# Kernel tuning notes

Measured on AMD Instinct MI355X. Metric: run time of the kernel, lower is better.

## Reference

```python
import jax, jax.numpy as jnp
import numpy as np

L, H, E, HS, T, B, V, BS = 12, 12, 768, 64, 1024, 4, 50257, 1024
EPS = 1e-8
SCALE = E ** -0.5  # NOTE: original code scales by n_embd**-0.5, not head_size**-0.5


def _ln(x, g, b):
    mu = jnp.mean(x, axis=-1, keepdims=True)
    var = jnp.mean((x - mu) ** 2, axis=-1, keepdims=True)
    return (x - mu) / jnp.sqrt(var + EPS) * g + b


def setup_inputs() -> dict:
    key = jax.random.key(0)
    ks = iter(jax.random.split(key, 32))
    s = 0.02
    inp = {
        "idx": jax.random.randint(next(ks), (B, T), 0, V, dtype=jnp.int64),
        "tok_emb": jax.random.normal(next(ks), (V, E), jnp.float32) * s,
        "pos_emb": jax.random.normal(next(ks), (BS, E), jnp.float32) * s,
        "wq": jax.random.normal(next(ks), (L, H, E, HS), jnp.float32) * s,
        "wk": jax.random.normal(next(ks), (L, H, E, HS), jnp.float32) * s,
        "wv": jax.random.normal(next(ks), (L, H, E, HS), jnp.float32) * s,
        "proj_w": jax.random.normal(next(ks), (L, E, E), jnp.float32) * s,
        "proj_b": jnp.zeros((L, E), jnp.float32),
        "ln1_g": jnp.ones((L, E), jnp.float32),
        "ln1_b": jnp.zeros((L, E), jnp.float32),
        "ln2_g": jnp.ones((L, E), jnp.float32),
        "ln2_b": jnp.zeros((L, E), jnp.float32),
        "w1": jax.random.normal(next(ks), (L, E, 4 * E), jnp.float32) * s,
        "b1": jnp.zeros((L, 4 * E), jnp.float32),
        "w2": jax.random.normal(next(ks), (L, 4 * E, E), jnp.float32) * s,
        "b2": jnp.zeros((L, E), jnp.float32),
        "lnf_g": jnp.ones((E,), jnp.float32),
        "lnf_b": jnp.zeros((E,), jnp.float32),
        "head_w": jax.random.normal(next(ks), (E, V), jnp.float32) * s,
        "head_b": jnp.zeros((V,), jnp.float32),
    }
    return inp


def reference(idx, tok_emb, pos_emb, wq, wk, wv, proj_w, proj_b,
              ln1_g, ln1_b, ln2_g, ln2_b, w1, b1, w2, b2,
              lnf_g, lnf_b, head_w, head_b):
    x = tok_emb[idx] + pos_emb[jnp.arange(T)][None, :, :]  # [B,T,E]
    mask = jnp.tril(jnp.ones((T, T), bool))
    neg = jnp.finfo(x.dtype).min
    for l in range(L):
        # --- multi-head attention ---
        xn = _ln(x, ln1_g[l], ln1_b[l])
        q = jnp.einsum("bte,hed->bhtd", xn, wq[l])
        k = jnp.einsum("bte,hed->bhtd", xn, wk[l])
        v = jnp.einsum("bte,hed->bhtd", xn, wv[l])
        scores = jnp.einsum("bhtd,bhsd->bhts", q, k) * SCALE
        scores = jnp.where(mask, scores, neg)
        attn = jax.nn.softmax(scores, axis=-1)
        o = jnp.einsum("bhts,bhsd->bhtd", attn, v)  # [B,H,T,HS]
        o = o.transpose(0, 2, 1, 3).reshape(B, T, E)
        x = x + o @ proj_w[l].T + proj_b[l]
        # --- feed-forward ---
        xn = _ln(x, ln2_g[l], ln2_b[l])
        h = jax.nn.gelu(xn @ w1[l] + b1[l], approximate=False)
        x = x + h @ w2[l] + b2[l]
    x = _ln(x, lnf_g, lnf_b)
    logits = x @ head_w + head_b  # [B,T,V]
    return logits
```

## Files before the change

### kernel.cpp

```cpp
#include <hip/hip_runtime.h>
#include <hip/hip_bf16.h>
#include <stdint.h>
#include <math.h>

typedef __hip_bfloat16 bf16;
typedef short s16x8 __attribute__((ext_vector_type(8)));
typedef short s16x4 __attribute__((ext_vector_type(4)));
typedef float f32x4 __attribute__((ext_vector_type(4)));

#define SCALE_QK 0.03608439182435161f
#define NEG_BIG  -1.0e30f

__device__ __forceinline__ void lds_dma16(void* lds_uniform, const void* gsrc) {
  __builtin_amdgcn_global_load_lds(
      (const __attribute__((address_space(1))) unsigned int*)(uintptr_t)gsrc,
      (__attribute__((address_space(3))) unsigned int*)(unsigned int)(uintptr_t)lds_uniform,
      16, 0, 0);
}

enum { EPI_BF16 = 0, EPI_GELU = 1, EPI_RES = 2, EPI_HEAD = 3 };

template <int EPI>
__global__ __launch_bounds__(256)
void gemm_bt(const bf16* __restrict__ A, const bf16* __restrict__ BT,
             const float* __restrict__ bias, float* Cf, bf16* Cb,
             int M, int N, int K, int Nreal)
{
  __shared__ __align__(16) bf16 As[2][128 * 32];
  __shared__ __align__(16) bf16 Bs[2][128 * 32];
  const int tid = threadIdx.x;
  const int w = tid >> 6, l = tid & 63;
  const int lo = l & 15, hi = l >> 4;
  const int wm = (w & 1) * 64, wn = (w >> 1) * 64;
  const long row0 = (long)blockIdx.y * 128;
  const long col0 = (long)blockIdx.x * 128;

  const int c0 = w * 64 + l, c1 = c0 + 256;
  const bf16* a0 = A + (row0 + (c0 >> 2)) * K + (c0 & 3) * 8;
  const bf16* a1 = A + (row0 + (c1 >> 2)) * K + (c1 & 3) * 8;
  const bf16* b0 = BT + (col0 + (c0 >> 2)) * K + (c0 & 3) * 8;
  const bf16* b1 = BT + (col0 + (c1 >> 2)) * K + (c1 & 3) * 8;
  const int w512 = w * 512;

  const f32x4 zero4 = {0.f, 0.f, 0.f, 0.f};
  f32x4 acc[4][4];
#pragma unroll
  for (int m = 0; m < 4; ++m)
#pragma unroll
    for (int n = 0; n < 4; ++n) acc[m][n] = zero4;

  const int nk = K >> 5;
  lds_dma16(&As[0][w512],        a0);
  lds_dma16(&As[0][2048 + w512], a1);
  lds_dma16(&Bs[0][w512],        b0);
  lds_dma16(&Bs[0][2048 + w512], b1);
  __syncthreads();

  int cur = 0;
  for (int t = 0; t < nk; ++t) {
    if (t + 1 < nk) {
      const int kt = (t + 1) << 5;
      lds_dma16(&As[cur ^ 1][w512],        a0 + kt);
      lds_dma16(&As[cur ^ 1][2048 + w512], a1 + kt);
      lds_dma16(&Bs[cur ^ 1][w512],        b0 + kt);
      lds_dma16(&Bs[cur ^ 1][2048 + w512], b1 + kt);
    }
    s16x8 af[4], bfr[4];
#pragma unroll
    for (int m = 0; m < 4; ++m)
      af[m] = *(const s16x8*)&As[cur][(wm + m * 16 + lo) * 32 + hi * 8];
#pragma unroll
    for (int n = 0; n < 4; ++n)
      bfr[n] = *(const s16x8*)&Bs[cur][(wn + n * 16 + lo) * 32 + hi * 8];
#pragma unroll
    for (int m = 0; m < 4; ++m)
#pragma unroll
      for (int n = 0; n < 4; ++n)
        acc[m][n] = __builtin_amdgcn_mfma_f32_16x16x32_bf16(af[m], bfr[n], acc[m][n], 0, 0, 0);
    __syncthreads();
    cur ^= 1;
  }

#pragma unroll
  for (int m = 0; m < 4; ++m) {
#pragma unroll
    for (int n = 0; n < 4; ++n) {
      const long col = col0 + wn + n * 16 + lo;
#pragma unroll
      for (int r = 0; r < 4; ++r) {
        const long row = row0 + wm + m * 16 + hi * 4 + r;
        float v = acc[m][n][r];
        if constexpr (EPI == EPI_BF16) {
          Cb[row * N + col] = __float2bfloat16(v);
        } else if constexpr (EPI == EPI_GELU) {
          v += bias[col];
          v = 0.5f * v * (1.f + erff(v * 0.70710678118654752f));
          Cb[row * N + col] = __float2bfloat16(v);
        } else if constexpr (EPI == EPI_RES) {
          Cf[row * N + col] += v + bias[col];
        } else {
          if (col < Nreal) Cf[row * Nreal + col] = v + bias[col];
        }
      }
    }
  }
}

__global__ __launch_bounds__(512)
void gemm_head256(const bf16* __restrict__ A, const bf16* __restrict__ BT,
                  const float* __restrict__ bias, float* __restrict__ Cf,
                  int K, int Nreal)
{
  __shared__ __align__(16) bf16 As[2][256 * 32];
  __shared__ __align__(16) bf16 Bs[2][128 * 32];
  const int tid = threadIdx.x;
  const int w = tid >> 6, l = tid & 63;
  const int lo = l & 15, hi = l >> 4;
  const int wm = (w & 3) * 64, wn = (w >> 2) * 64;
  const long row0 = (long)blockIdx.y * 256;
  const long col0 = (long)blockIdx.x * 128;

  const bf16* a0 = A + (row0 + (tid >> 2)) * K + (tid & 3) * 8;
  const bf16* a1 = A + (row0 + 128 + (tid >> 2)) * K + (tid & 3) * 8;
  const bf16* b0 = BT + (col0 + (tid >> 2)) * K + (tid & 3) * 8;
  const int w512 = w * 512;

  const f32x4 zero4 = {0.f, 0.f, 0.f, 0.f};
  f32x4 acc[4][4];
#pragma unroll
  for (int m = 0; m < 4; ++m)
#pragma unroll
    for (int n = 0; n < 4; ++n) acc[m][n] = zero4;

  const int nk = K >> 5;
  lds_dma16(&As[0][w512],        a0);
  lds_dma16(&As[0][4096 + w512], a1);
  lds_dma16(&Bs[0][w512],        b0);
  __syncthreads();

  int cur = 0;
  for (int t = 0; t < nk; ++t) {
    if (t + 1 < nk) {
      const int kt = (t + 1) << 5;
      lds_dma16(&As[cur ^ 1][w512],        a0 + kt);
      lds_dma16(&As[cur ^ 1][4096 + w512], a1 + kt);
      lds_dma16(&Bs[cur ^ 1][w512],        b0 + kt);
    }
    s16x8 af[4], bfr[4];
#pragma unroll
    for (int m = 0; m < 4; ++m)
      af[m] = *(const s16x8*)&As[cur][(wm + m * 16 + lo) * 32 + hi * 8];
#pragma unroll
    for (int n = 0; n < 4; ++n)
      bfr[n] = *(const s16x8*)&Bs[cur][(wn + n * 16 + lo) * 32 + hi * 8];
#pragma unroll
    for (int m = 0; m < 4; ++m)
#pragma unroll
      for (int n = 0; n < 4; ++n)
        acc[m][n] = __builtin_amdgcn_mfma_f32_16x16x32_bf16(af[m], bfr[n], acc[m][n], 0, 0, 0);
    __syncthreads();
    cur ^= 1;
  }

#pragma unroll
  for (int m = 0; m < 4; ++m) {
#pragma unroll
    for (int n = 0; n < 4; ++n) {
      const long col = col0 + wn + n * 16 + lo;
#pragma unroll
      for (int r = 0; r < 4; ++r) {
        const long row = row0 + wm + m * 16 + hi * 4 + r;
        if (col < Nreal)
          Cf[row * Nreal + col] = acc[m][n][r] + bias[col];
      }
    }
  }
}

__global__ __launch_bounds__(256)
void attn_kernel(const bf16* __restrict__ qkv, bf16* __restrict__ o)
{
  __shared__ __align__(16) bf16 Kl[64 * 64];
  __shared__ __align__(16) bf16 Vl[64 * 64];
  __shared__ __align__(16) bf16 Pl[4][32 * 64];
  const int tid = threadIdx.x;
  const int w = tid >> 6, l = tid & 63;
  const int lo = l & 15, hi = l >> 4;
  const int q0 = blockIdx.x * 128;
  const int b = blockIdx.y / 12, h = blockIdx.y % 12;
  const int wq0 = q0 + w * 32;
  const bf16* base = qkv + (long)b * 1024 * 2304;

  s16x8 qf[2][2];
#pragma unroll
  for (int m = 0; m < 2; ++m)
#pragma unroll
    for (int ks = 0; ks < 2; ++ks)
      qf[m][ks] = *(const s16x8*)(base + (long)(wq0 + m * 16 + lo) * 2304 + h * 64 + ks * 32 + hi * 8);

  const f32x4 zero4 = {0.f, 0.f, 0.f, 0.f};
  f32x4 oacc[2][4];
  float mst[2][4], lst[2][4];
#pragma unroll
  for (int m = 0; m < 2; ++m) {
#pragma unroll
    for (int n = 0; n < 4; ++n) oacc[m][n] = zero4;
#pragma unroll
    for (int r = 0; r < 4; ++r) { mst[m][r] = -3.0e38f; lst[m][r] = 0.f; }
  }

  const int cB = tid + 256;

  const int nt = (q0 + 128) / 64;
  for (int t = 0; t < nt; ++t) {
    const int j0 = t * 64;
    const s16x8 rk0 = *(const s16x8*)(base + (long)(j0 + (tid >> 3)) * 2304 +  768 + h * 64 + (tid & 7) * 8);
    const s16x8 rk1 = *(const s16x8*)(base + (long)(j0 + (cB  >> 3)) * 2304 +  768 + h * 64 + (cB  & 7) * 8);
    const s16x8 rv0 = *(const s16x8*)(base + (long)(j0 + (tid >> 3)) * 2304 + 1536 + h * 64 + (tid & 7) * 8);
    const s16x8 rv1 = *(const s16x8*)(base + (long)(j0 + (cB  >> 3)) * 2304 + 1536 + h * 64 + (cB  & 7) * 8);
    __syncthreads();
    *(s16x8*)&Kl[tid * 8] = rk0;
    *(s16x8*)&Kl[cB  * 8] = rk1;
    *(s16x8*)&Vl[tid * 8] = rv0;
    *(s16x8*)&Vl[cB  * 8] = rv1;
    __syncthreads();

    if (j0 <= wq0 + 31) {
      f32x4 s[2][4];
#pragma unroll
      for (int m = 0; m < 2; ++m)
#pragma unroll
        for (int n = 0; n < 4; ++n) s[m][n] = zero4;
#pragma unroll
      for (int ks = 0; ks < 2; ++ks) {
        s16x8 kf[4];
#pragma unroll
        for (int n = 0; n < 4; ++n)
          kf[n] = *(const s16x8*)&Kl[(n * 16 + lo) * 64 + ks * 32 + hi * 8];
#pragma unroll
        for (int m = 0; m < 2; ++m)
#pragma unroll
          for (int n = 0; n < 4; ++n)
            s[m][n] = __builtin_amdgcn_mfma_f32_16x16x32_bf16(qf[m][ks], kf[n], s[m][n], 0, 0, 0);
      }
      const bool edge = (j0 + 63 > wq0);
#pragma unroll
      for (int m = 0; m < 2; ++m)
#pragma unroll
        for (int n = 0; n < 4; ++n) {
          const int j = j0 + n * 16 + lo;
#pragma unroll
          for (int r = 0; r < 4; ++r) {
            float v = s[m][n][r] * SCALE_QK;
            if (edge && j > wq0 + m * 16 + hi * 4 + r) v = NEG_BIG;
            s[m][n][r] = v;
          }
        }
#pragma unroll
      for (int m = 0; m < 2; ++m)
#pragma unroll
        for (int r = 0; r < 4; ++r) {
          float x = fmaxf(fmaxf(s[m][0][r], s[m][1][r]), fmaxf(s[m][2][r], s[m][3][r]));
          x = fmaxf(x, __shfl_xor(x, 1));
          x = fmaxf(x, __shfl_xor(x, 2));
          x = fmaxf(x, __shfl_xor(x, 4));
          x = fmaxf(x, __shfl_xor(x, 8));
          const float mn = fmaxf(mst[m][r], x);
          const float corr = __expf(mst[m][r] - mn);
          mst[m][r] = mn;
          float rs = 0.f;
#pragma unroll
          for (int n = 0; n < 4; ++n) {
            float p = __expf(s[m][n][r] - mn);
            s[m][n][r] = p;
            rs += p;
          }
          rs += __shfl_xor(rs, 1);
          rs += __shfl_xor(rs, 2);
          rs += __shfl_xor(rs, 4);
          rs += __shfl_xor(rs, 8);
          lst[m][r] = lst[m][r] * corr + rs;
#pragma unroll
          for (int n = 0; n < 4; ++n) oacc[m][n][r] *= corr;
        }
#pragma unroll
      for (int m = 0; m < 2; ++m)
#pragma unroll
        for (int n = 0; n < 4; ++n)
#pragma unroll
          for (int r = 0; r < 4; ++r)
            Pl[w][(m * 16 + hi * 4 + r) * 64 + n * 16 + lo] = __float2bfloat16(s[m][n][r]);
      s16x8 pa[2][2];
#pragma unroll
      for (int m = 0; m < 2; ++m)
#pragma unroll
        for (int ks = 0; ks < 2; ++ks)
          pa[m][ks] = *(const s16x8*)&Pl[w][(m * 16 + lo) * 64 + ks * 32 + hi * 8];
#pragma unroll
      for (int ks = 0; ks < 2; ++ks)
#pragma unroll
        for (int n = 0; n < 4; ++n) {
          s16x8 vf;
#pragma unroll
          for (int j = 0; j < 8; ++j)
            vf[j] = *(const short*)&Vl[(ks * 32 + hi * 8 + j) * 64 + n * 16 + lo];
#pragma unroll
          for (int m = 0; m < 2; ++m)
            oacc[m][n] = __builtin_amdgcn_mfma_f32_16x16x32_bf16(pa[m][ks], vf, oacc[m][n], 0, 0, 0);
        }
    }
  }
#pragma unroll
  for (int m = 0; m < 2; ++m)
#pragma unroll
    for (int n = 0; n < 4; ++n)
#pragma unroll
      for (int r = 0; r < 4; ++r) {
        const int q = wq0 + m * 16 + hi * 4 + r;
        o[(long)(b * 1024 + q) * 768 + h * 64 + n * 16 + lo] =
            __float2bfloat16(oacc[m][n][r] / lst[m][r]);
      }
}

__global__ void detect_idx(const int* __restrict__ idx, int* __restrict__ flag)
{
  const int t = threadIdx.x;
  const int v = idx[2 * t + 1];
  const unsigned long long nz = __ballot(v != 0);
  if (t == 0) flag[0] = (nz == 0ull) ? 1 : 0;
}

__global__ __launch_bounds__(192)
void embed_kernel(const int* __restrict__ idx, const float* __restrict__ tok,
                  const float* __restrict__ pos, float* __restrict__ x,
                  const int* __restrict__ flag)
{
  const int row = blockIdx.x;
  const int t = row & 1023;
  const int id = flag[0] ? idx[2 * row] : idx[row];
  const int e = threadIdx.x * 4;
  const float4 a = *(const float4*)&tok[(long)id * 768 + e];
  const float4 p = *(const float4*)&pos[(long)t * 768 + e];
  float4 r; r.x = a.x + p.x; r.y = a.y + p.y; r.z = a.z + p.z; r.w = a.w + p.w;
  *(float4*)&x[(long)row * 768 + e] = r;
}

__global__ __launch_bounds__(256)
void ln_kernel(const float* __restrict__ x, const float* __restrict__ g,
               const float* __restrict__ bt, bf16* __restrict__ out)
{
  const int lane = threadIdx.x & 63;
  const int row = blockIdx.x * 4 + (threadIdx.x >> 6);
  const float* xr = x + (long)row * 768;
  f32x4 v[3];
  float s = 0.f, q = 0.f;
#pragma unroll
  for (int p = 0; p < 3; ++p) {
    v[p] = *(const f32x4*)&xr[lane * 4 + p * 256];
#pragma unroll
    for (int j = 0; j < 4; ++j) { s += v[p][j]; q += v[p][j] * v[p][j]; }
  }
#pragma unroll
  for (int o = 32; o > 0; o >>= 1) { s += __shfl_xor(s, o); q += __shfl_xor(q, o); }
  const float mu = s * (1.f / 768.f);
  const float var = q * (1.f / 768.f) - mu * mu;
  const float rs = rsqrtf(var + 1e-8f);
  bf16* orow = out + (long)row * 768;
#pragma unroll
  for (int p = 0; p < 3; ++p) {
    const int e = lane * 4 + p * 256;
    s16x4 pk;
#pragma unroll
    for (int j = 0; j < 4; ++j) {
      bf16 t = __float2bfloat16((v[p][j] - mu) * rs * g[e + j] + bt[e + j]);
      pk[j] = *(const short*)&t;
    }
    *(s16x4*)&orow[e] = pk;
  }
}

__device__ __forceinline__ void tile_tr64(const float* __restrict__ ip,
                                          bf16* __restrict__ op,
                                          int R, int Creal, int r0, int c0,
                                          int tid, float (*tile)[65])
{
  const int tx = tid & 63, ty = tid >> 6;
#pragma unroll
  for (int p = 0; p < 16; ++p) {
    const int r = p * 4 + ty;
    const int c = c0 + tx;
    tile[r][tx] = (c < Creal) ? ip[(long)(r0 + r) * Creal + c] : 0.f;
  }
  __syncthreads();
#pragma unroll
  for (int p = 0; p < 16; ++p) {
    const int cc = p * 4 + ty;
    op[(long)(c0 + cc) * R + r0 + tx] = __float2bfloat16(tile[tx][cc]);
  }
}

__global__ __launch_bounds__(256)
void transpose_conv(const float* __restrict__ in, bf16* __restrict__ out,
                    int R, int Creal)
{
  __shared__ float tile[64][65];
  tile_tr64(in, out, R, Creal, blockIdx.y * 64, blockIdx.x * 64, threadIdx.x, tile);
}

__global__ __launch_bounds__(256)
void repack_layer(const float* __restrict__ wq, const float* __restrict__ wk,
                  const float* __restrict__ wv, const float* __restrict__ projw,
                  const float* __restrict__ w1, const float* __restrict__ w2,
                  bf16* __restrict__ WqkvT, bf16* __restrict__ WprojT,
                  bf16* __restrict__ W1T, bf16* __restrict__ W2T)
{
  __shared__ float tile[64][65];
  const int tid = threadIdx.x;
  const int t = blockIdx.x;
  if (t < 432) {
    const int op_i = t / 144, r = t % 144;
    const int h = r / 12, ry = r % 12;
    const float* ip = (op_i == 0 ? wq : op_i == 1 ? wk : wv) + h * 49152;
    bf16* op = WqkvT + (long)op_i * 768 * 768 + (long)h * 64 * 768;
    tile_tr64(ip, op, 768, 64, ry * 64, 0, tid, tile);
  } else if (t < 576) {
    const int t2 = t - 432;
    const int r0 = (t2 / 12) * 64, c0 = (t2 % 12) * 64;
#pragma unroll
    for (int p = 0; p < 4; ++p) {
      const int row = r0 + p * 16 + (tid >> 4);
      const int col = c0 + (tid & 15) * 4;
      const float4 v = *(const float4*)&projw[(long)row * 768 + col];
      bf16 t0 = __float2bfloat16(v.x), t1 = __float2bfloat16(v.y);
      bf16 t2b = __float2bfloat16(v.z), t3 = __float2bfloat16(v.w);
      s16x4 pk;
      pk[0] = *(const short*)&t0; pk[1] = *(const short*)&t1;
      pk[2] = *(const short*)&t2b; pk[3] = *(const short*)&t3;
      *(s16x4*)&WprojT[(long)row * 768 + col] = pk;
    }
  } else if (t < 1152) {
    const int t3 = t - 576;
    tile_tr64(w1, W1T, 768, 3072, (t3 / 48) * 64, (t3 % 48) * 64, tid, tile);
  } else {
    const int t4 = t - 1152;
    tile_tr64(w2, W2T, 3072, 768, (t4 / 12) * 64, (t4 % 12) * 64, tid, tile);
  }
}

extern "C" void kernel_launch(void* const* d_in, const int* in_sizes, int n_in,
                              void* d_out, int out_size, void* d_ws, size_t ws_size,
                              hipStream_t stream)
{
  (void)in_sizes; (void)n_in; (void)out_size; (void)ws_size;
  const int*   idx   = (const int*)d_in[0];
  const float* tok   = (const float*)d_in[1];
  const float* pos   = (const float*)d_in[2];
  const float* wq    = (const float*)d_in[3];
  const float* wk    = (const float*)d_in[4];
  const float* wv    = (const float*)d_in[5];
  const float* projw = (const float*)d_in[6];
  const float* projb = (const float*)d_in[7];
  const float* ln1g  = (const float*)d_in[8];
  const float* ln1b  = (const float*)d_in[9];
  const float* ln2g  = (const float*)d_in[10];
  const float* ln2b  = (const float*)d_in[11];
  const float* w1    = (const float*)d_in[12];
  const float* b1    = (const float*)d_in[13];
  const float* w2    = (const float*)d_in[14];
  const float* b2    = (const float*)d_in[15];
  const float* lnfg  = (const float*)d_in[16];
  const float* lnfb  = (const float*)d_in[17];
  const float* headw = (const float*)d_in[18];
  const float* headb = (const float*)d_in[19];
  float* out = (float*)d_out;

  char* ws = (char*)d_ws;
  size_t off = 0;
  auto alloc = [&](size_t bytes) -> void* {
    void* p = ws + off; off += (bytes + 255) & ~(size_t)255; return p;
  };
  int*   iflag  = (int*)  alloc(256);
  float* x      = (float*)alloc(4096ull * 768 * 4);
  bf16*  xn     = (bf16*) alloc(4096ull * 768 * 2);
  bf16*  qkvb   = (bf16*) alloc(4096ull * 2304 * 2);
  bf16*  ob     = (bf16*) alloc(4096ull * 768 * 2);
  bf16*  hb     = (bf16*) alloc(4096ull * 3072 * 2);
  bf16*  WqkvT  = (bf16*) alloc(2304ull * 768 * 2);
  bf16*  WprojT = (bf16*) alloc(768ull * 768 * 2);
  bf16*  W1T    = (bf16*) alloc(3072ull * 768 * 2);
  bf16*  W2T    = (bf16*) alloc(768ull * 3072 * 2);
  bf16*  headT  = (bf16*) alloc(50304ull * 768 * 2);

  detect_idx<<<1, 64, 0, stream>>>(idx, iflag);
  transpose_conv<<<dim3(786, 12), 256, 0, stream>>>(headw, headT, 768, 50257);
  embed_kernel<<<4096, 192, 0, stream>>>(idx, tok, pos, x, iflag);

  for (int l = 0; l < 12; ++l) {
    const size_t hOff = (size_t)l * 12 * 768 * 64;
    repack_layer<<<1728, 256, 0, stream>>>(wq + hOff, wk + hOff, wv + hOff,
                                           projw + (size_t)l * 768 * 768,
                                           w1 + (size_t)l * 768 * 3072,
                                           w2 + (size_t)l * 3072 * 768,
                                           WqkvT, WprojT, W1T, W2T);

    ln_kernel<<<1024, 256, 0, stream>>>(x, ln1g + l * 768, ln1b + l * 768, xn);
    gemm_bt<EPI_BF16><<<dim3(18, 32), 256, 0, stream>>>(xn, WqkvT, nullptr, nullptr, qkvb, 4096, 2304, 768, 2304);
    attn_kernel<<<dim3(8, 48), 256, 0, stream>>>(qkvb, ob);
    gemm_bt<EPI_RES><<<dim3(6, 32), 256, 0, stream>>>(ob, WprojT, projb + l * 768, x, nullptr, 4096, 768, 768, 768);
    ln_kernel<<<1024, 256, 0, stream>>>(x, ln2g + l * 768, ln2b + l * 768, xn);
    gemm_bt<EPI_GELU><<<dim3(24, 32), 256, 0, stream>>>(xn, W1T, b1 + (size_t)l * 3072, nullptr, hb, 4096, 3072, 768, 3072);
    gemm_bt<EPI_RES><<<dim3(6, 32), 256, 0, stream>>>(hb, W2T, b2 + l * 768, x, nullptr, 4096, 768, 3072, 768);
  }

  ln_kernel<<<1024, 256, 0, stream>>>(x, lnfg, lnfb, xn);
  gemm_head256<<<dim3(393, 16), 512, 0, stream>>>(xn, headT, headb, out, 768, 50257);
}
```

Baseline: 3.625 ms.

## Batch all-layer weight repacking into one launch and prefetch attention K/V tiles

Replaces the twelve per-layer weight repack launches with a single 2D-grid launch that converts and transposes all layers' weights up front into per-layer workspace slices. This removes launch overhead and lets the repack work run as one large parallel kernel, at the cost of about 12x more workspace for the bf16 weights. It also software-pipelines the attention kernel by loading the next K/V tile into registers while the current tile is being computed, hiding global-load latency at some extra register cost.

```diff
diff --git a/kernel.cpp b/kernel.cpp
--- a/kernel.cpp
+++ b/kernel.cpp
@@ -210,20 +210,33 @@
   }
 
   const int cB = tid + 256;
+  const bf16* ksrc0 = base + (long)(tid >> 3) * 2304 +  768 + h * 64 + (tid & 7) * 8;
+  const bf16* ksrc1 = base + (long)(cB  >> 3) * 2304 +  768 + h * 64 + (cB  & 7) * 8;
+  const bf16* vsrc0 = ksrc0 + 768;
+  const bf16* vsrc1 = ksrc1 + 768;
+  const long jstride = 2304;
 
   const int nt = (q0 + 128) / 64;
+  s16x8 rk0 = *(const s16x8*)(ksrc0);
+  s16x8 rk1 = *(const s16x8*)(ksrc1);
+  s16x8 rv0 = *(const s16x8*)(vsrc0);
+  s16x8 rv1 = *(const s16x8*)(vsrc1);
+
   for (int t = 0; t < nt; ++t) {
     const int j0 = t * 64;
-    const s16x8 rk0 = *(const s16x8*)(base + (long)(j0 + (tid >> 3)) * 2304 +  768 + h * 64 + (tid & 7) * 8);
-    const s16x8 rk1 = *(const s16x8*)(base + (long)(j0 + (cB  >> 3)) * 2304 +  768 + h * 64 + (cB  & 7) * 8);
-    const s16x8 rv0 = *(const s16x8*)(base + (long)(j0 + (tid >> 3)) * 2304 + 1536 + h * 64 + (tid & 7) * 8);
-    const s16x8 rv1 = *(const s16x8*)(base + (long)(j0 + (cB  >> 3)) * 2304 + 1536 + h * 64 + (cB  & 7) * 8);
     __syncthreads();
     *(s16x8*)&Kl[tid * 8] = rk0;
     *(s16x8*)&Kl[cB  * 8] = rk1;
     *(s16x8*)&Vl[tid * 8] = rv0;
     *(s16x8*)&Vl[cB  * 8] = rv1;
     __syncthreads();
+    if (t + 1 < nt) {
+      const long jo = (long)(j0 + 64) * jstride;
+      rk0 = *(const s16x8*)(ksrc0 + jo);
+      rk1 = *(const s16x8*)(ksrc1 + jo);
+      rv0 = *(const s16x8*)(vsrc0 + jo);
+      rv1 = *(const s16x8*)(vsrc1 + jo);
+    }
 
     if (j0 <= wq0 + 31) {
       f32x4 s[2][4];
@@ -408,20 +421,32 @@
 }
 
 __global__ __launch_bounds__(256)
-void repack_layer(const float* __restrict__ wq, const float* __restrict__ wk,
-                  const float* __restrict__ wv, const float* __restrict__ projw,
-                  const float* __restrict__ w1, const float* __restrict__ w2,
-                  bf16* __restrict__ WqkvT, bf16* __restrict__ WprojT,
-                  bf16* __restrict__ W1T, bf16* __restrict__ W2T)
+void repack_all(const float* __restrict__ wq, const float* __restrict__ wk,
+                const float* __restrict__ wv, const float* __restrict__ projw,
+                const float* __restrict__ w1, const float* __restrict__ w2,
+                bf16* __restrict__ WqkvT, bf16* __restrict__ WprojT,
+                bf16* __restrict__ W1T, bf16* __restrict__ W2T)
 {
   __shared__ float tile[64][65];
   const int tid = threadIdx.x;
   const int t = blockIdx.x;
+  const int lyr = blockIdx.y;
+  const float* wq_l    = wq    + (size_t)lyr * 12 * 768 * 64;
+  const float* wk_l    = wk    + (size_t)lyr * 12 * 768 * 64;
+  const float* wv_l    = wv    + (size_t)lyr * 12 * 768 * 64;
+  const float* projw_l = projw + (size_t)lyr * 768 * 768;
+  const float* w1_l    = w1    + (size_t)lyr * 768 * 3072;
+  const float* w2_l    = w2    + (size_t)lyr * 3072 * 768;
+  bf16* WqkvT_l  = WqkvT  + (size_t)lyr * 2304 * 768;
+  bf16* WprojT_l = WprojT + (size_t)lyr * 768 * 768;
+  bf16* W1T_l    = W1T    + (size_t)lyr * 3072 * 768;
+  bf16* W2T_l    = W2T    + (size_t)lyr * 768 * 3072;
+
   if (t < 432) {
     const int op_i = t / 144, r = t % 144;
     const int h = r / 12, ry = r % 12;
-    const float* ip = (op_i == 0 ? wq : op_i == 1 ? wk : wv) + h * 49152;
-    bf16* op = WqkvT + (long)op_i * 768 * 768 + (long)h * 64 * 768;
+    const float* ip = (op_i == 0 ? wq_l : op_i == 1 ? wk_l : wv_l) + h * 49152;
+    bf16* op = WqkvT_l + (long)op_i * 768 * 768 + (long)h * 64 * 768;
     tile_tr64(ip, op, 768, 64, ry * 64, 0, tid, tile);
   } else if (t < 576) {
     const int t2 = t - 432;
@@ -430,20 +455,20 @@
     for (int p = 0; p < 4; ++p) {
       const int row = r0 + p * 16 + (tid >> 4);
       const int col = c0 + (tid & 15) * 4;
-      const float4 v = *(const float4*)&projw[(long)row * 768 + col];
+      const float4 v = *(const float4*)&projw_l[(long)row * 768 + col];
       bf16 t0 = __float2bfloat16(v.x), t1 = __float2bfloat16(v.y);
       bf16 t2b = __float2bfloat16(v.z), t3 = __float2bfloat16(v.w);
       s16x4 pk;
       pk[0] = *(const short*)&t0; pk[1] = *(const short*)&t1;
       pk[2] = *(const short*)&t2b; pk[3] = *(const short*)&t3;
-      *(s16x4*)&WprojT[(long)row * 768 + col] = pk;
+      *(s16x4*)&WprojT_l[(long)row * 768 + col] = pk;
     }
   } else if (t < 1152) {
     const int t3 = t - 576;
-    tile_tr64(w1, W1T, 768, 3072, (t3 / 48) * 64, (t3 % 48) * 64, tid, tile);
+    tile_tr64(w1_l, W1T_l, 768, 3072, (t3 / 48) * 64, (t3 % 48) * 64, tid, tile);
   } else {
     const int t4 = t - 1152;
-    tile_tr64(w2, W2T, 3072, 768, (t4 / 12) * 64, (t4 % 12) * 64, tid, tile);
+    tile_tr64(w2_l, W2T_l, 3072, 768, (t4 / 12) * 64, (t4 % 12) * 64, tid, tile);
   }
 }
 
@@ -485,31 +510,31 @@
   bf16*  qkvb   = (bf16*) alloc(4096ull * 2304 * 2);
   bf16*  ob     = (bf16*) alloc(4096ull * 768 * 2);
   bf16*  hb     = (bf16*) alloc(4096ull * 3072 * 2);
-  bf16*  WqkvT  = (bf16*) alloc(2304ull * 768 * 2);
-  bf16*  WprojT = (bf16*) alloc(768ull * 768 * 2);
-  bf16*  W1T    = (bf16*) alloc(3072ull * 768 * 2);
-  bf16*  W2T    = (bf16*) alloc(768ull * 3072 * 2);
+  bf16*  WqkvT  = (bf16*) alloc(12ull * 2304 * 768 * 2);
+  bf16*  WprojT = (bf16*) alloc(12ull * 768 * 768 * 2);
+  bf16*  W1T    = (bf16*) alloc(12ull * 3072 * 768 * 2);
+  bf16*  W2T    = (bf16*) alloc(12ull * 768 * 3072 * 2);
   bf16*  headT  = (bf16*) alloc(50304ull * 768 * 2);
 
   detect_idx<<<1, 64, 0, stream>>>(idx, iflag);
+  repack_all<<<dim3(1728, 12), 256, 0, stream>>>(wq, wk, wv, projw, w1, w2,
+                                                 WqkvT, WprojT, W1T, W2T);
   transpose_conv<<<dim3(786, 12), 256, 0, stream>>>(headw, headT, 768, 50257);
   embed_kernel<<<4096, 192, 0, stream>>>(idx, tok, pos, x, iflag);
 
   for (int l = 0; l < 12; ++l) {
-    const size_t hOff = (size_t)l * 12 * 768 * 64;
-    repack_layer<<<1728, 256, 0, stream>>>(wq + hOff, wk + hOff, wv + hOff,
-                                           projw + (size_t)l * 768 * 768,
-                                           w1 + (size_t)l * 768 * 3072,
-                                           w2 + (size_t)l * 3072 * 768,
-                                           WqkvT, WprojT, W1T, W2T);
+    const bf16* WqkvT_l  = WqkvT  + (size_t)l * 2304 * 768;
+    const bf16* WprojT_l = WprojT + (size_t)l * 768 * 768;
+    const bf16* W1T_l    = W1T    + (size_t)l * 3072 * 768;
+    const bf16* W2T_l    = W2T    + (size_t)l * 768 * 3072;
 
     ln_kernel<<<1024, 256, 0, stream>>>(x, ln1g + l * 768, ln1b + l * 768, xn);
-    gemm_bt<EPI_BF16><<<dim3(18, 32), 256, 0, stream>>>(xn, WqkvT, nullptr, nullptr, qkvb, 4096, 2304, 768, 2304);
+    gemm_bt<EPI_BF16><<<dim3(18, 32), 256, 0, stream>>>(xn, WqkvT_l, nullptr, nullptr, qkvb, 4096, 2304, 768, 2304);
     attn_kernel<<<dim3(8, 48), 256, 0, stream>>>(qkvb, ob);
-    gemm_bt<EPI_RES><<<dim3(6, 32), 256, 0, stream>>>(ob, WprojT, projb + l * 768, x, nullptr, 4096, 768, 768, 768);
+    gemm_bt<EPI_RES><<<dim3(6, 32), 256, 0, stream>>>(ob, WprojT_l, projb + l * 768, x, nullptr, 4096, 768, 768, 768);
     ln_kernel<<<1024, 256, 0, stream>>>(x, ln2g + l * 768, ln2b + l * 768, xn);
-    gemm_bt<EPI_GELU><<<dim3(24, 32), 256, 0, stream>>>(xn, W1T, b1 + (size_t)l * 3072, nullptr, hb, 4096, 3072, 768, 3072);
-    gemm_bt<EPI_RES><<<dim3(6, 32), 256, 0, stream>>>(hb, W2T, b2 + l * 768, x, nullptr, 4096, 768, 3072, 768);
+    gemm_bt<EPI_GELU><<<dim3(24, 32), 256, 0, stream>>>(xn, W1T_l, b1 + (size_t)l * 3072, nullptr, hb, 4096, 3072, 768, 3072);
+    gemm_bt<EPI_RES><<<dim3(6, 32), 256, 0, stream>>>(hb, W2T_l, b2 + l * 768, x, nullptr, 4096, 768, 3072, 768);
   }
 
   ln_kernel<<<1024, 256, 0, stream>>>(x, lnfg, lnfb, xn);
```

New measurement: 3.729 ms. +2.9%, slower.
